# Kernel tuning notes

Measured on AMD Instinct MI355X. Metric: run time of the kernel, lower is better.

The kernel has to match this reference:

```python
import jax, jax.numpy as jnp
import numpy as np

N = 131072
IN, HID, OUT = 128, 256, 64
NUM_TASKS = 16
NUM_COPIES = 4
NUM_LAYERS = 3


def setup_inputs() -> dict:
    key = jax.random.key(0)
    ks = jax.random.split(key, 10)
    inputs = jax.random.normal(ks[0], (N, IN), dtype=jnp.float32)
    task_indices = jax.random.randint(ks[1], (N,), 0, NUM_TASKS, dtype=jnp.int32)
    copy_maps = jax.random.randint(ks[2], (NUM_LAYERS, NUM_TASKS), 0, NUM_COPIES, dtype=jnp.int32)
    # per-copy Linear weights, Kaiming-ish scale 1/sqrt(fan_in)
    W0 = jax.random.normal(ks[3], (NUM_COPIES, IN, HID), dtype=jnp.float32) / np.sqrt(IN)
    b0 = jax.random.normal(ks[4], (NUM_COPIES, HID), dtype=jnp.float32) * 0.01
    W1 = jax.random.normal(ks[5], (NUM_COPIES, HID, HID), dtype=jnp.float32) / np.sqrt(HID)
    b1 = jax.random.normal(ks[6], (NUM_COPIES, HID), dtype=jnp.float32) * 0.01
    W2 = jax.random.normal(ks[7], (NUM_COPIES, HID, OUT), dtype=jnp.float32) / np.sqrt(HID)
    b2 = jax.random.normal(ks[8], (NUM_COPIES, OUT), dtype=jnp.float32) * 0.01
    return {"inputs": inputs, "task_indices": task_indices, "copy_maps": copy_maps,
            "W0": W0, "b0": b0, "W1": W1, "b1": b1, "W2": W2, "b2": b2}


def _routed_layer(x, W, b, copy_idx, apply_tanh):
    # x: [N, d_in], W: [C, d_in, d_out], b: [C, d_out], copy_idx: [N]
    # Each token goes through exactly one copy's Linear. Equivalent to the
    # torch sort->per-copy-forward->unsort, expressed as masked accumulation
    # over the small fixed set of copies (avoids data-dependent shapes).
    y = jnp.zeros((x.shape[0], W.shape[2]), dtype=x.dtype)
    for c in range(W.shape[0]):
        mask = (copy_idx == c).astype(x.dtype)[:, None]  # [N, 1]
        y = y + mask * (x @ W[c] + b[c])
    return jnp.tanh(y) if apply_tanh else y


def reference(inputs, task_indices, copy_maps, W0, b0, W1, b1, W2, b2):
    x = inputs
    Ws = (W0, W1, W2)
    bs = (b0, b1, b2)
    for layer in range(NUM_LAYERS):
        copy_idx = copy_maps[layer][task_indices]  # [N] task->copy routing
        x = _routed_layer(x, Ws[layer], bs[layer], copy_idx,
                          apply_tanh=(layer != NUM_LAYERS - 1))
    return x
```

## Files before the change

### kernel.cpp

```cpp
#include <hip/hip_runtime.h>

#define N_TOK 131072
#define TILE 64
#define NT_MAX 2064

typedef __attribute__((ext_vector_type(8))) short s8v;
typedef __attribute__((ext_vector_type(4))) float f4v;
typedef unsigned short ushort_t;

__device__ __forceinline__ unsigned short f2bf(float x) {
    union { float f; unsigned u; } v; v.f = x;
    unsigned r = v.u + 0x7fffu + ((v.u >> 16) & 1u);
    return (unsigned short)(r >> 16);
}

__device__ __forceinline__ unsigned pk2(float a, float b) {
    union { float f; unsigned u; } x, y; x.f = a; y.f = b;
    return __byte_perm(x.u + 0x8000u, y.u + 0x8000u, 0x7632);
}

__device__ __forceinline__ float tanh_fast(float x) {
    float e = __expf(2.0f * x);
    float r = __builtin_amdgcn_rcpf(e + 1.0f);
    return __builtin_fmaf(-2.0f, r, 1.0f);
}

__global__ void prep_hist_kernel(const float* __restrict__ W0, const float* __restrict__ W1,
                                 const float* __restrict__ W2,
                                 ushort_t* __restrict__ W0p, ushort_t* __restrict__ W1p,
                                 ushort_t* __restrict__ W2p,
                                 const int* __restrict__ task, int* __restrict__ blockCounts) {
    if (blockIdx.x < 224) {
        int f = blockIdx.x * 256 + threadIdx.x;
        const float* src; ushort_t* dst; int K, N;
        if (f < 16384)      { src = W0; dst = W0p; K = 128; N = 256; }
        else if (f < 49152) { src = W1; dst = W1p; K = 256; N = 256; f -= 16384; }
        else                { src = W2; dst = W2p; K = 256; N = 64;  f -= 49152; }
        int fpc = (N >> 4) * (K >> 5) * 64;
        int c = f / fpc, r = f % fpc;
        int lane = r & 63;
        int kt = (r >> 6) % (K >> 5);
        int ftile = (r >> 6) / (K >> 5);
        int n = ftile * 16 + (lane & 15);
        int kbase = kt * 32 + (lane >> 4) * 8;
        const float* s = src + (size_t)c * K * N + (size_t)kbase * N + n;
        s8v pk;
#pragma unroll
        for (int j = 0; j < 8; j++) pk[j] = (short)f2bf(s[(size_t)j * N]);
        *reinterpret_cast<s8v*>(dst + ((size_t)(c * fpc + r) << 3)) = pk;
    } else {
        __shared__ int cnt[16];
        int t = threadIdx.x;
        int hb = blockIdx.x - 224;
        if (t < 16) cnt[t] = 0;
        __syncthreads();
        int base = hb * 2048 + t;
#pragma unroll
        for (int i = 0; i < 8; i++) atomicAdd(&cnt[task[base + i * 256]], 1);
        __syncthreads();
        if (t < 16) blockCounts[hb * 16 + t] = cnt[t];
    }
}

__global__ void sort_kernel(const int* __restrict__ task, const int* __restrict__ blockCounts,
                            int* __restrict__ tileTask, int* __restrict__ nT,
                            int* __restrict__ perm) {
    __shared__ int cntLds[1024];
    __shared__ int total[16], pref[16], rank[16];
    __shared__ int tokBase[16], tbase[17];
    int t = threadIdx.x, b = blockIdx.x;
    for (int i = t; i < 1024; i += 256) cntLds[i] = blockCounts[i];
    if (t < 16) rank[t] = 0;
    __syncthreads();
    if (t < 16) {
        int tot = 0, pf = 0;
#pragma unroll
        for (int bb = 0; bb < 64; bb++) {
            int v = cntLds[bb * 16 + t];
            tot += v;
            if (bb < b) pf += v;
        }
        total[t] = tot; pref[t] = pf;
    }
    __syncthreads();
    if (t == 0) {
        int tok = 0, tile = 0;
        for (int k = 0; k < 16; k++) {
            tokBase[k] = tok;
            tbase[k] = tile;
            int ntk = (total[k] + TILE - 1) / TILE;
            tok += ntk * TILE;
            tile += ntk;
        }
        tbase[16] = tile;
        if (b == 0) nT[0] = tile;
    }
    __syncthreads();
    if (b == 0) {
        for (int i = t; i < NT_MAX; i += 256) {
            int tk = 0;
            if (i < tbase[16]) {
#pragma unroll
                for (int k = 0; k < 16; k++) if (i >= tbase[k]) tk = k;
            }
            tileTask[i] = tk;
        }
        for (int i = t; i < 16 * TILE; i += 256) {
            int k = i >> 6, off = i & (TILE - 1);
            int idx = total[k] + off;
            int lim = ((total[k] + TILE - 1) / TILE) * TILE;
            if (idx < lim) perm[tokBase[k] + idx] = -1;
        }
    }
    int tk[8], my[8];
#pragma unroll
    for (int i = 0; i < 8; i++) {
        int idx = b * 2048 + i * 256 + t;
        tk[i] = task[idx];
        my[i] = atomicAdd(&rank[tk[i]], 1);
    }
#pragma unroll
    for (int i = 0; i < 8; i++) {
        int idx = b * 2048 + i * 256 + t;
        perm[tokBase[tk[i]] + pref[tk[i]] + my[i]] = idx;
    }
}

__launch_bounds__(512, 4)
__global__ void mlp_kernel(const float* __restrict__ x_in,
                           const int* __restrict__ cmap,
                           const float* __restrict__ b0,
                           const float* __restrict__ b1,
                           const float* __restrict__ b2,
                           const ushort_t* __restrict__ W0p,
                           const ushort_t* __restrict__ W1p,
                           const ushort_t* __restrict__ W2p,
                           const int* __restrict__ tileTask,
                           const int* __restrict__ nTp,
                           const int* __restrict__ perm,
                           float* __restrict__ out) {
    __shared__ __align__(16) ushort_t H1[16384];
    __shared__ __align__(16) ushort_t XH2[16384];

    int b = blockIdx.x;
    if (b >= nTp[0]) return;
    int t = threadIdx.x;
    int task = tileTask[b];
    int c0 = cmap[task], c1 = cmap[16 + task], c2 = cmap[32 + task];

    int w = t >> 6;
    int lane = t & 63;
    int l15 = lane & 15, lq = lane >> 4;

    {
        int r = t >> 3, q = t & 7;
        int tok = perm[b * TILE + r];
        float4 v0 = make_float4(0.f, 0.f, 0.f, 0.f), v1 = v0, v2 = v0, v3 = v0;
        if ((unsigned)tok < (unsigned)N_TOK) {
            const float4* src = reinterpret_cast<const float4*>(x_in) + (size_t)tok * 32 + q * 4;
            v0 = src[0]; v1 = src[1]; v2 = src[2]; v3 = src[3];
        }
        int fragid = (r >> 4) * 4 + (q >> 1);
        int lp0 = (r & 15) + 16 * ((q & 1) * 2);
        uint4 pk0, pk1;
        pk0.x = pk2(v0.x, v0.y); pk0.y = pk2(v0.z, v0.w);
        pk0.z = pk2(v1.x, v1.y); pk0.w = pk2(v1.z, v1.w);
        pk1.x = pk2(v2.x, v2.y); pk1.y = pk2(v2.z, v2.w);
        pk1.z = pk2(v3.x, v3.y); pk1.w = pk2(v3.z, v3.w);
        *reinterpret_cast<uint4*>(&XH2[(fragid * 64 + lp0) << 3]) = pk0;
        *reinterpret_cast<uint4*>(&XH2[(fragid * 64 + lp0 + 16) << 3]) = pk1;
    }
    __syncthreads();

    {
        f4v acc[2][4];
#pragma unroll
        for (int mi = 0; mi < 2; mi++) {
            float4 bv = *reinterpret_cast<const float4*>(b0 + c0 * 256 + (2 * w + mi) * 16 + lq * 4);
#pragma unroll
            for (int nt = 0; nt < 4; nt++) {
                acc[mi][nt][0] = bv.x; acc[mi][nt][1] = bv.y;
                acc[mi][nt][2] = bv.z; acc[mi][nt][3] = bv.w;
            }
        }
        const ushort_t* Wc = W0p + (size_t)c0 * 32768;
#pragma unroll
        for (int kt = 0; kt < 4; kt++) {
            s8v wa[2];
#pragma unroll
            for (int mi = 0; mi < 2; mi++)
                wa[mi] = *reinterpret_cast<const s8v*>(Wc + ((((2 * w + mi) * 4 + kt) * 64 + lane) << 3));
            s8v xb[4];
#pragma unroll
            for (int nt = 0; nt < 4; nt++)
                xb[nt] = *reinterpret_cast<const s8v*>(&XH2[((nt * 4 + kt) * 64 + lane) << 3]);
#pragma unroll
            for (int mi = 0; mi < 2; mi++)
#pragma unroll
                for (int nt = 0; nt < 4; nt++)
                    acc[mi][nt] = __builtin_amdgcn_mfma_f32_16x16x32_bf16(wa[mi], xb[nt], acc[mi][nt], 0, 0, 0);
        }
#pragma unroll
        for (int mi = 0; mi < 2; mi++) {
            int ft = 2 * w + mi;
            int kt_h = ft >> 1;
            int lanep = l15 + 16 * ((ft & 1) * 2 + (lq >> 1));
            int j0 = (lq & 1) * 4;
#pragma unroll
            for (int nt = 0; nt < 4; nt++) {
                float t0 = tanh_fast(acc[mi][nt][0]);
                float t1 = tanh_fast(acc[mi][nt][1]);
                float t2 = tanh_fast(acc[mi][nt][2]);
                float t3 = tanh_fast(acc[mi][nt][3]);
                uint2 pk; pk.x = pk2(t0, t1); pk.y = pk2(t2, t3);
                *reinterpret_cast<uint2*>(&H1[(((nt * 8 + kt_h) * 64 + lanep) << 3) + j0]) = pk;
            }
        }
    }
    __syncthreads();

    {
        f4v acc[2][4];
#pragma unroll
        for (int mi = 0; mi < 2; mi++) {
            float4 bv = *reinterpret_cast<const float4*>(b1 + c1 * 256 + (2 * w + mi) * 16 + lq * 4);
#pragma unroll
            for (int nt = 0; nt < 4; nt++) {
                acc[mi][nt][0] = bv.x; acc[mi][nt][1] = bv.y;
                acc[mi][nt][2] = bv.z; acc[mi][nt][3] = bv.w;
            }
        }
        const ushort_t* Wc = W1p + (size_t)c1 * 65536;
#pragma unroll
        for (int kt = 0; kt < 8; kt++) {
            s8v wa[2];
#pragma unroll
            for (int mi = 0; mi < 2; mi++)
                wa[mi] = *reinterpret_cast<const s8v*>(Wc + ((((2 * w + mi) * 8 + kt) * 64 + lane) << 3));
            s8v xb[4];
#pragma unroll
            for (int nt = 0; nt < 4; nt++)
                xb[nt] = *reinterpret_cast<const s8v*>(&H1[((nt * 8 + kt) * 64 + lane) << 3]);
#pragma unroll
            for (int mi = 0; mi < 2; mi++)
#pragma unroll
                for (int nt = 0; nt < 4; nt++)
                    acc[mi][nt] = __builtin_amdgcn_mfma_f32_16x16x32_bf16(wa[mi], xb[nt], acc[mi][nt], 0, 0, 0);
        }
#pragma unroll
        for (int mi = 0; mi < 2; mi++) {
            int ft = 2 * w + mi;
            int kt_h = ft >> 1;
            int lanep = l15 + 16 * ((ft & 1) * 2 + (lq >> 1));
            int j0 = (lq & 1) * 4;
#pragma unroll
            for (int nt = 0; nt < 4; nt++) {
                float t0 = tanh_fast(acc[mi][nt][0]);
                float t1 = tanh_fast(acc[mi][nt][1]);
                float t2 = tanh_fast(acc[mi][nt][2]);
                float t3 = tanh_fast(acc[mi][nt][3]);
                uint2 pk; pk.x = pk2(t0, t1); pk.y = pk2(t2, t3);
                *reinterpret_cast<uint2*>(&XH2[(((nt * 8 + kt_h) * 64 + lanep) << 3) + j0]) = pk;
            }
        }
    }
    __syncthreads();

    {
        int mt = w & 3, ntb = (w >> 2) * 2;
        float4 bv = *reinterpret_cast<const float4*>(b2 + c2 * 64 + mt * 16 + lq * 4);
        f4v acc[2];
#pragma unroll
        for (int e = 0; e < 2; e++) {
            acc[e][0] = bv.x; acc[e][1] = bv.y; acc[e][2] = bv.z; acc[e][3] = bv.w;
        }
        const ushort_t* Wc = W2p + (size_t)c2 * 16384;
#pragma unroll
        for (int kt = 0; kt < 8; kt++) {
            s8v wa = *reinterpret_cast<const s8v*>(Wc + (((mt * 8 + kt) * 64 + lane) << 3));
#pragma unroll
            for (int e = 0; e < 2; e++) {
                s8v xb = *reinterpret_cast<const s8v*>(&XH2[(((ntb + e) * 8 + kt) * 64 + lane) << 3]);
                acc[e] = __builtin_amdgcn_mfma_f32_16x16x32_bf16(wa, xb, acc[e], 0, 0, 0);
            }
        }
#pragma unroll
        for (int e = 0; e < 2; e++) {
            int nt = ntb + e;
            int tok = perm[b * TILE + nt * 16 + l15];
            if ((unsigned)tok < (unsigned)N_TOK) {
                float4 o;
                o.x = acc[e][0]; o.y = acc[e][1]; o.z = acc[e][2]; o.w = acc[e][3];
                *reinterpret_cast<float4*>(out + (size_t)tok * 64 + mt * 16 + lq * 4) = o;
            }
        }
    }
}

extern "C" void kernel_launch(void* const* d_in, const int* in_sizes, int n_in,
                              void* d_out, int out_size, void* d_ws, size_t ws_size,
                              hipStream_t stream) {
    const float* inputs = (const float*)d_in[0];
    const int*   task   = (const int*)d_in[1];
    const int*   cmap   = (const int*)d_in[2];
    const float* W0     = (const float*)d_in[3];
    const float* b0     = (const float*)d_in[4];
    const float* W1     = (const float*)d_in[5];
    const float* b1     = (const float*)d_in[6];
    const float* W2     = (const float*)d_in[7];
    const float* b2     = (const float*)d_in[8];
    float* out = (float*)d_out;

    char* ws = (char*)d_ws;
    int* blockCounts = (int*)(ws + 0);
    int* nT          = (int*)(ws + 4096);
    int* tileTask    = (int*)(ws + 4160);
    int* perm        = (int*)(ws + 12416);
    ushort_t* W0p    = (ushort_t*)(ws + 540800);
    ushort_t* W1p    = (ushort_t*)(ws + 802944);
    ushort_t* W2p    = (ushort_t*)(ws + 1327232);

    prep_hist_kernel<<<288, 256, 0, stream>>>(W0, W1, W2, W0p, W1p, W2p, task, blockCounts);
    sort_kernel<<<64, 256, 0, stream>>>(task, blockCounts, tileTask, nT, perm);
    mlp_kernel<<<NT_MAX, 512, 0, stream>>>(inputs, cmap, b0, b1, b2,
                                           W0p, W1p, W2p, tileTask, nT, perm, out);
}
```

Baseline: 162.2 us.

## Make MLP kernel persistent per task with register-resident weights and prefetch

The MLP kernel changes from one block per 64-token tile to 256 persistent blocks, 16 per task, each looping over that task's tiles with stride 16. All three layers' weight fragments and biases are loaded into registers once per block, and the next tile's input rows are prefetched while the current tile is being computed. The sort kernel now writes only per-task tile bases instead of a per-tile task table. This removes repeated weight reloads from global/L2 for every tile, at the cost of many more registers (launch bounds lowered to 2 blocks per CU) and possible load imbalance across tasks of unequal size.

```diff
diff --git a/kernel.cpp b/kernel.cpp
--- a/kernel.cpp
+++ b/kernel.cpp
@@ -3,6 +3,7 @@
 #define N_TOK 131072
 #define TILE 64
 #define NT_MAX 2064
+#define NBLK 256
 
 typedef __attribute__((ext_vector_type(8))) short s8v;
 typedef __attribute__((ext_vector_type(4))) float f4v;
@@ -63,8 +64,7 @@
 }
 
 __global__ void sort_kernel(const int* __restrict__ task, const int* __restrict__ blockCounts,
-                            int* __restrict__ tileTask, int* __restrict__ nT,
-                            int* __restrict__ perm) {
+                            int* __restrict__ tbaseG, int* __restrict__ perm) {
     __shared__ int cntLds[1024];
     __shared__ int total[16], pref[16], rank[16];
     __shared__ int tokBase[16], tbase[17];
@@ -93,18 +93,10 @@
             tile += ntk;
         }
         tbase[16] = tile;
-        if (b == 0) nT[0] = tile;
     }
     __syncthreads();
     if (b == 0) {
-        for (int i = t; i < NT_MAX; i += 256) {
-            int tk = 0;
-            if (i < tbase[16]) {
-#pragma unroll
-                for (int k = 0; k < 16; k++) if (i >= tbase[k]) tk = k;
-            }
-            tileTask[i] = tk;
-        }
+        if (t < 17) tbaseG[t] = tbase[t];
         for (int i = t; i < 16 * TILE; i += 256) {
             int k = i >> 6, off = i & (TILE - 1);
             int idx = total[k] + off;
@@ -126,7 +118,7 @@
     }
 }
 
-__launch_bounds__(512, 4)
+__launch_bounds__(512, 2)
 __global__ void mlp_kernel(const float* __restrict__ x_in,
                            const int* __restrict__ cmap,
                            const float* __restrict__ b0,
@@ -135,165 +127,202 @@
                            const ushort_t* __restrict__ W0p,
                            const ushort_t* __restrict__ W1p,
                            const ushort_t* __restrict__ W2p,
-                           const int* __restrict__ tileTask,
-                           const int* __restrict__ nTp,
+                           const int* __restrict__ tbaseG,
                            const int* __restrict__ perm,
                            float* __restrict__ out) {
     __shared__ __align__(16) ushort_t H1[16384];
     __shared__ __align__(16) ushort_t XH2[16384];
 
-    int b = blockIdx.x;
-    if (b >= nTp[0]) return;
+    int p = blockIdx.x;
+    int k = p >> 4, sub = p & 15;
+    int tBeg = tbaseG[k], tEnd = tbaseG[k + 1];
+    if (tBeg + sub >= tEnd) return;
+
     int t = threadIdx.x;
-    int task = tileTask[b];
-    int c0 = cmap[task], c1 = cmap[16 + task], c2 = cmap[32 + task];
+    int c0 = cmap[k], c1 = cmap[16 + k], c2 = cmap[32 + k];
 
     int w = t >> 6;
     int lane = t & 63;
     int l15 = lane & 15, lq = lane >> 4;
-
+    int mt2 = w & 3, ntb2 = (w >> 2) * 2;
+
+    s8v wa0[2][4], wa1[2][8], wa2r[8];
     {
-        int r = t >> 3, q = t & 7;
-        int tok = perm[b * TILE + r];
-        float4 v0 = make_float4(0.f, 0.f, 0.f, 0.f), v1 = v0, v2 = v0, v3 = v0;
-        if ((unsigned)tok < (unsigned)N_TOK) {
-            const float4* src = reinterpret_cast<const float4*>(x_in) + (size_t)tok * 32 + q * 4;
+        const ushort_t* Wc = W0p + (size_t)c0 * 32768;
+#pragma unroll
+        for (int mi = 0; mi < 2; mi++)
+#pragma unroll
+            for (int kt = 0; kt < 4; kt++)
+                wa0[mi][kt] = *reinterpret_cast<const s8v*>(Wc + ((((2 * w + mi) * 4 + kt) * 64 + lane) << 3));
+    }
+    {
+        const ushort_t* Wc = W1p + (size_t)c1 * 65536;
+#pragma unroll
+        for (int mi = 0; mi < 2; mi++)
+#pragma unroll
+            for (int kt = 0; kt < 8; kt++)
+                wa1[mi][kt] = *reinterpret_cast<const s8v*>(Wc + ((((2 * w + mi) * 8 + kt) * 64 + lane) << 3));
+    }
+    {
+        const ushort_t* Wc = W2p + (size_t)c2 * 16384;
+#pragma unroll
+        for (int kt = 0; kt < 8; kt++)
+            wa2r[kt] = *reinterpret_cast<const s8v*>(Wc + (((mt2 * 8 + kt) * 64 + lane) << 3));
+    }
+    float4 bv0[2], bv1[2], bv2;
+#pragma unroll
+    for (int mi = 0; mi < 2; mi++) {
+        bv0[mi] = *reinterpret_cast<const float4*>(b0 + c0 * 256 + (2 * w + mi) * 16 + lq * 4);
+        bv1[mi] = *reinterpret_cast<const float4*>(b1 + c1 * 256 + (2 * w + mi) * 16 + lq * 4);
+    }
+    bv2 = *reinterpret_cast<const float4*>(b2 + c2 * 64 + mt2 * 16 + lq * 4);
+
+    int r = t >> 3, q = t & 7;
+    const float4* xbase = reinterpret_cast<const float4*>(x_in);
+    float4 v0 = make_float4(0.f, 0.f, 0.f, 0.f), v1 = v0, v2 = v0, v3 = v0;
+    int ptok = -1;
+
+    int tile = tBeg + sub;
+    {
+        ptok = perm[tile * TILE + r];
+        if ((unsigned)ptok < (unsigned)N_TOK) {
+            const float4* src = xbase + (size_t)ptok * 32 + q * 4;
             v0 = src[0]; v1 = src[1]; v2 = src[2]; v3 = src[3];
         }
-        int fragid = (r >> 4) * 4 + (q >> 1);
-        int lp0 = (r & 15) + 16 * ((q & 1) * 2);
-        uint4 pk0, pk1;
-        pk0.x = pk2(v0.x, v0.y); pk0.y = pk2(v0.z, v0.w);
-        pk0.z = pk2(v1.x, v1.y); pk0.w = pk2(v1.z, v1.w);
-        pk1.x = pk2(v2.x, v2.y); pk1.y = pk2(v2.z, v2.w);
-        pk1.z = pk2(v3.x, v3.y); pk1.w = pk2(v3.z, v3.w);
-        *reinterpret_cast<uint4*>(&XH2[(fragid * 64 + lp0) << 3]) = pk0;
-        *reinterpret_cast<uint4*>(&XH2[(fragid * 64 + lp0 + 16) << 3]) = pk1;
-    }
-    __syncthreads();
-
-    {
-        f4v acc[2][4];
-#pragma unroll
-        for (int mi = 0; mi < 2; mi++) {
-            float4 bv = *reinterpret_cast<const float4*>(b0 + c0 * 256 + (2 * w + mi) * 16 + lq * 4);
-#pragma unroll
-            for (int nt = 0; nt < 4; nt++) {
-                acc[mi][nt][0] = bv.x; acc[mi][nt][1] = bv.y;
-                acc[mi][nt][2] = bv.z; acc[mi][nt][3] = bv.w;
-            }
-        }
-        const ushort_t* Wc = W0p + (size_t)c0 * 32768;
-#pragma unroll
-        for (int kt = 0; kt < 4; kt++) {
-            s8v wa[2];
+    }
+
+    for (; tile < tEnd; tile += 16) {
+        {
+            int fragid = (r >> 4) * 4 + (q >> 1);
+            int lp0 = (r & 15) + 16 * ((q & 1) * 2);
+            uint4 pk0, pk1;
+            pk0.x = pk2(v0.x, v0.y); pk0.y = pk2(v0.z, v0.w);
+            pk0.z = pk2(v1.x, v1.y); pk0.w = pk2(v1.z, v1.w);
+            pk1.x = pk2(v2.x, v2.y); pk1.y = pk2(v2.z, v2.w);
+            pk1.z = pk2(v3.x, v3.y); pk1.w = pk2(v3.z, v3.w);
+            *reinterpret_cast<uint4*>(&XH2[(fragid * 64 + lp0) << 3]) = pk0;
+            *reinterpret_cast<uint4*>(&XH2[(fragid * 64 + lp0 + 16) << 3]) = pk1;
+        }
+        int ntile = tile + 16;
+        if (ntile < tEnd) {
+            ptok = perm[ntile * TILE + r];
+            float4 z = make_float4(0.f, 0.f, 0.f, 0.f);
+            float4 a0 = z, a1 = z, a2 = z, a3 = z;
+            if ((unsigned)ptok < (unsigned)N_TOK) {
+                const float4* src = xbase + (size_t)ptok * 32 + q * 4;
+                a0 = src[0]; a1 = src[1]; a2 = src[2]; a3 = src[3];
+            }
+            v0 = a0; v1 = a1; v2 = a2; v3 = a3;
+        }
+        __syncthreads();
+
+        {
+            f4v acc[2][4];
 #pragma unroll
             for (int mi = 0; mi < 2; mi++)
-                wa[mi] = *reinterpret_cast<const s8v*>(Wc + ((((2 * w + mi) * 4 + kt) * 64 + lane) << 3));
-            s8v xb[4];
-#pragma unroll
-            for (int nt = 0; nt < 4; nt++)
-                xb[nt] = *reinterpret_cast<const s8v*>(&XH2[((nt * 4 + kt) * 64 + lane) << 3]);
+#pragma unroll
+                for (int nt = 0; nt < 4; nt++) {
+                    acc[mi][nt][0] = bv0[mi].x; acc[mi][nt][1] = bv0[mi].y;
+                    acc[mi][nt][2] = bv0[mi].z; acc[mi][nt][3] = bv0[mi].w;
+                }
+#pragma unroll
+            for (int kt = 0; kt < 4; kt++) {
+                s8v xb[4];
+#pragma unroll
+                for (int nt = 0; nt < 4; nt++)
+                    xb[nt] = *reinterpret_cast<const s8v*>(&XH2[((nt * 4 + kt) * 64 + lane) << 3]);
+#pragma unroll
+                for (int mi = 0; mi < 2; mi++)
+#pragma unroll
+                    for (int nt = 0; nt < 4; nt++)
+                        acc[mi][nt] = __builtin_amdgcn_mfma_f32_16x16x32_bf16(wa0[mi][kt], xb[nt], acc[mi][nt], 0, 0, 0);
+            }
+#pragma unroll
+            for (int mi = 0; mi < 2; mi++) {
+                int ft = 2 * w + mi;
+                int kt_h = ft >> 1;
+                int lanep = l15 + 16 * ((ft & 1) * 2 + (lq >> 1));
+                int j0 = (lq & 1) * 4;
+#pragma unroll
+                for (int nt = 0; nt < 4; nt++) {
+                    float t0 = tanh_fast(acc[mi][nt][0]);
+                    float t1 = tanh_fast(acc[mi][nt][1]);
+                    float t2 = tanh_fast(acc[mi][nt][2]);
+                    float t3 = tanh_fast(acc[mi][nt][3]);
+                    uint2 pk; pk.x = pk2(t0, t1); pk.y = pk2(t2, t3);
+                    *reinterpret_cast<uint2*>(&H1[(((nt * 8 + kt_h) * 64 + lanep) << 3) + j0]) = pk;
+                }
+            }
+        }
+        __syncthreads();
+
+        {
+            f4v acc[2][4];
 #pragma unroll
             for (int mi = 0; mi < 2; mi++)
 #pragma unroll
+                for (int nt = 0; nt < 4; nt++) {
+                    acc[mi][nt][0] = bv1[mi].x; acc[mi][nt][1] = bv1[mi].y;
+                    acc[mi][nt][2] = bv1[mi].z; acc[mi][nt][3] = bv1[mi].w;
+                }
+#pragma unroll
+            for (int kt = 0; kt < 8; kt++) {
+                s8v xb[4];
+#pragma unroll
                 for (int nt = 0; nt < 4; nt++)
-                    acc[mi][nt] = __builtin_amdgcn_mfma_f32_16x16x32_bf16(wa[mi], xb[nt], acc[mi][nt], 0, 0, 0);
-        }
-#pragma unroll
-        for (int mi = 0; mi < 2; mi++) {
-            int ft = 2 * w + mi;
-            int kt_h = ft >> 1;
-            int lanep = l15 + 16 * ((ft & 1) * 2 + (lq >> 1));
-            int j0 = (lq & 1) * 4;
-#pragma unroll
-            for (int nt = 0; nt < 4; nt++) {
-                float t0 = tanh_fast(acc[mi][nt][0]);
-                float t1 = tanh_fast(acc[mi][nt][1]);
-                float t2 = tanh_fast(acc[mi][nt][2]);
-                float t3 = tanh_fast(acc[mi][nt][3]);
-                uint2 pk; pk.x = pk2(t0, t1); pk.y = pk2(t2, t3);
-                *reinterpret_cast<uint2*>(&H1[(((nt * 8 + kt_h) * 64 + lanep) << 3) + j0]) = pk;
-            }
-        }
-    }
-    __syncthreads();
-
-    {
-        f4v acc[2][4];
-#pragma unroll
-        for (int mi = 0; mi < 2; mi++) {
-            float4 bv = *reinterpret_cast<const float4*>(b1 + c1 * 256 + (2 * w + mi) * 16 + lq * 4);
-#pragma unroll
-            for (int nt = 0; nt < 4; nt++) {
-                acc[mi][nt][0] = bv.x; acc[mi][nt][1] = bv.y;
-                acc[mi][nt][2] = bv.z; acc[mi][nt][3] = bv.w;
-            }
-        }
-        const ushort_t* Wc = W1p + (size_t)c1 * 65536;
-#pragma unroll
-        for (int kt = 0; kt < 8; kt++) {
-            s8v wa[2];
-#pragma unroll
-            for (int mi = 0; mi < 2; mi++)
-                wa[mi] = *reinterpret_cast<const s8v*>(Wc + ((((2 * w + mi) * 8 + kt) * 64 + lane) << 3));
-            s8v xb[4];
-#pragma unroll
-            for (int nt = 0; nt < 4; nt++)
-                xb[nt] = *reinterpret_cast<const s8v*>(&H1[((nt * 8 + kt) * 64 + lane) << 3]);
-#pragma unroll
-            for (int mi = 0; mi < 2; mi++)
-#pragma unroll
-                for (int nt = 0; nt < 4; nt++)
-                    acc[mi][nt] = __builtin_amdgcn_mfma_f32_16x16x32_bf16(wa[mi], xb[nt], acc[mi][nt], 0, 0, 0);
-        }
-#pragma unroll
-        for (int mi = 0; mi < 2; mi++) {
-            int ft = 2 * w + mi;
-            int kt_h = ft >> 1;
-            int lanep = l15 + 16 * ((ft & 1) * 2 + (lq >> 1));
-            int j0 = (lq & 1) * 4;
-#pragma unroll
-            for (int nt = 0; nt < 4; nt++) {
-                float t0 = tanh_fast(acc[mi][nt][0]);
-                float t1 = tanh_fast(acc[mi][nt][1]);
-                float t2 = tanh_fast(acc[mi][nt][2]);
-                float t3 = tanh_fast(acc[mi][nt][3]);
-                uint2 pk; pk.x = pk2(t0, t1); pk.y = pk2(t2, t3);
-                *reinterpret_cast<uint2*>(&XH2[(((nt * 8 + kt_h) * 64 + lanep) << 3) + j0]) = pk;
-            }
-        }
-    }
-    __syncthreads();
-
-    {
-        int mt = w & 3, ntb = (w >> 2) * 2;
-        float4 bv = *reinterpret_cast<const float4*>(b2 + c2 * 64 + mt * 16 + lq * 4);
-        f4v acc[2];
-#pragma unroll
-        for (int e = 0; e < 2; e++) {
-            acc[e][0] = bv.x; acc[e][1] = bv.y; acc[e][2] = bv.z; acc[e][3] = bv.w;
-        }
-        const ushort_t* Wc = W2p + (size_t)c2 * 16384;
-#pragma unroll
-        for (int kt = 0; kt < 8; kt++) {
-            s8v wa = *reinterpret_cast<const s8v*>(Wc + (((mt * 8 + kt) * 64 + lane) << 3));
+                    xb[nt] = *reinterpret_cast<const s8v*>(&H1[((nt * 8 + kt) * 64 + lane) << 3]);
+#pragma unroll
+                for (int mi = 0; mi < 2; mi++)
+#pragma unroll
+                    for (int nt = 0; nt < 4; nt++)
+                        acc[mi][nt] = __builtin_amdgcn_mfma_f32_16x16x32_bf16(wa1[mi][kt], xb[nt], acc[mi][nt], 0, 0, 0);
+            }
+#pragma unroll
+            for (int mi = 0; mi < 2; mi++) {
+                int ft = 2 * w + mi;
+                int kt_h = ft >> 1;
+                int lanep = l15 + 16 * ((ft & 1) * 2 + (lq >> 1));
+                int j0 = (lq & 1) * 4;
+#pragma unroll
+                for (int nt = 0; nt < 4; nt++) {
+                    float t0 = tanh_fast(acc[mi][nt][0]);
+                    float t1 = tanh_fast(acc[mi][nt][1]);
+                    float t2 = tanh_fast(acc[mi][nt][2]);
+                    float t3 = tanh_fast(acc[mi][nt][3]);
+                    uint2 pk; pk.x = pk2(t0, t1); pk.y = pk2(t2, t3);
+                    *reinterpret_cast<uint2*>(&XH2[(((nt * 8 + kt_h) * 64 + lanep) << 3) + j0]) = pk;
+                }
+            }
+        }
+        __syncthreads();
+
+        {
+            int tok0 = perm[tile * TILE + ntb2 * 16 + l15];
+            int tok1 = perm[tile * TILE + (ntb2 + 1) * 16 + l15];
+            f4v acc[2];
 #pragma unroll
             for (int e = 0; e < 2; e++) {
-                s8v xb = *reinterpret_cast<const s8v*>(&XH2[(((ntb + e) * 8 + kt) * 64 + lane) << 3]);
-                acc[e] = __builtin_amdgcn_mfma_f32_16x16x32_bf16(wa, xb, acc[e], 0, 0, 0);
-            }
-        }
-#pragma unroll
-        for (int e = 0; e < 2; e++) {
-            int nt = ntb + e;
-            int tok = perm[b * TILE + nt * 16 + l15];
-            if ((unsigned)tok < (unsigned)N_TOK) {
-                float4 o;
-                o.x = acc[e][0]; o.y = acc[e][1]; o.z = acc[e][2]; o.w = acc[e][3];
-                *reinterpret_cast<float4*>(out + (size_t)tok * 64 + mt * 16 + lq * 4) = o;
-            }
-        }
+                acc[e][0] = bv2.x; acc[e][1] = bv2.y; acc[e][2] = bv2.z; acc[e][3] = bv2.w;
+            }
+#pragma unroll
+            for (int kt = 0; kt < 8; kt++) {
+#pragma unroll
+                for (int e = 0; e < 2; e++) {
+                    s8v xb = *reinterpret_cast<const s8v*>(&XH2[(((ntb2 + e) * 8 + kt) * 64 + lane) << 3]);
+                    acc[e] = __builtin_amdgcn_mfma_f32_16x16x32_bf16(wa2r[kt], xb, acc[e], 0, 0, 0);
+                }
+            }
+#pragma unroll
+            for (int e = 0; e < 2; e++) {
+                int tok = e ? tok1 : tok0;
+                if ((unsigned)tok < (unsigned)N_TOK) {
+                    float4 o;
+                    o.x = acc[e][0]; o.y = acc[e][1]; o.z = acc[e][2]; o.w = acc[e][3];
+                    *reinterpret_cast<float4*>(out + (size_t)tok * 64 + mt2 * 16 + lq * 4) = o;
+                }
+            }
+        }
+        __syncthreads();
     }
 }
 
@@ -313,15 +342,14 @@
 
     char* ws = (char*)d_ws;
     int* blockCounts = (int*)(ws + 0);
-    int* nT          = (int*)(ws + 4096);
-    int* tileTask    = (int*)(ws + 4160);
-    int* perm        = (int*)(ws + 12416);
-    ushort_t* W0p    = (ushort_t*)(ws + 540800);
-    ushort_t* W1p    = (ushort_t*)(ws + 802944);
-    ushort_t* W2p    = (ushort_t*)(ws + 1327232);
+    int* tbaseG      = (int*)(ws + 4096);
+    int* perm        = (int*)(ws + 4224);
+    ushort_t* W0p    = (ushort_t*)(ws + 532608);
+    ushort_t* W1p    = (ushort_t*)(ws + 794752);
+    ushort_t* W2p    = (ushort_t*)(ws + 1319040);
 
     prep_hist_kernel<<<288, 256, 0, stream>>>(W0, W1, W2, W0p, W1p, W2p, task, blockCounts);
-    sort_kernel<<<64, 256, 0, stream>>>(task, blockCounts, tileTask, nT, perm);
-    mlp_kernel<<<NT_MAX, 512, 0, stream>>>(inputs, cmap, b0, b1, b2,
-                                           W0p, W1p, W2p, tileTask, nT, perm, out);
-}
+    sort_kernel<<<64, 256, 0, stream>>>(task, blockCounts, tbaseG, perm);
+    mlp_kernel<<<NBLK, 512, 0, stream>>>(inputs, cmap, b0, b1, b2,
+                                         W0p, W1p, W2p, tbaseG, perm, out);
+}
```

Result: no change. 160.5 us (-1.0%).

## Double token tile to 128 per block to halve weight refetches

Applied to the files above, without the earlier changes.

Raises the token tile from 64 to 128 rows per block, doubling the per-warp MFMA column tiles and LDS buffers to 64 KB each, and lowers launch bounds occupancy to 2. Each block now reuses every weight fragment across twice as many tokens, cutting global weight traffic and block count. It also switches tanh to use exp2 with a prescaled argument. The costs are higher register and LDS pressure, lower occupancy, and more padding waste per task segment.

```diff
diff --git a/kernel.cpp b/kernel.cpp
--- a/kernel.cpp
+++ b/kernel.cpp
@@ -1,8 +1,8 @@
 #include <hip/hip_runtime.h>
 
 #define N_TOK 131072
-#define TILE 64
-#define NT_MAX 2064
+#define TILE 128
+#define NT_MAX 1040
 
 typedef __attribute__((ext_vector_type(8))) short s8v;
 typedef __attribute__((ext_vector_type(4))) float f4v;
@@ -20,7 +20,7 @@
 }
 
 __device__ __forceinline__ float tanh_fast(float x) {
-    float e = __expf(2.0f * x);
+    float e = __builtin_amdgcn_exp2f(x * 2.8853900817779268f);
     float r = __builtin_amdgcn_rcpf(e + 1.0f);
     return __builtin_fmaf(-2.0f, r, 1.0f);
 }
@@ -106,7 +106,7 @@
             tileTask[i] = tk;
         }
         for (int i = t; i < 16 * TILE; i += 256) {
-            int k = i >> 6, off = i & (TILE - 1);
+            int k = i >> 7, off = i & (TILE - 1);
             int idx = total[k] + off;
             int lim = ((total[k] + TILE - 1) / TILE) * TILE;
             if (idx < lim) perm[tokBase[k] + idx] = -1;
@@ -126,7 +126,7 @@
     }
 }
 
-__launch_bounds__(512, 4)
+__launch_bounds__(512, 2)
 __global__ void mlp_kernel(const float* __restrict__ x_in,
                            const int* __restrict__ cmap,
                            const float* __restrict__ b0,
@@ -139,8 +139,8 @@
                            const int* __restrict__ nTp,
                            const int* __restrict__ perm,
                            float* __restrict__ out) {
-    __shared__ __align__(16) ushort_t H1[16384];
-    __shared__ __align__(16) ushort_t XH2[16384];
+    __shared__ __align__(16) ushort_t H1[32768];
+    __shared__ __align__(16) ushort_t XH2[32768];
 
     int b = blockIdx.x;
     if (b >= nTp[0]) return;
@@ -151,54 +151,54 @@
     int w = t >> 6;
     int lane = t & 63;
     int l15 = lane & 15, lq = lane >> 4;
+    int mt2 = w & 3, ntb2 = (w >> 2) * 4;
+
+    const ushort_t* Wc0 = W0p + (size_t)c0 * 32768;
+    const ushort_t* Wc1 = W1p + (size_t)c1 * 65536;
+    const ushort_t* Wc2 = W2p + (size_t)c2 * 16384;
 
     {
-        int r = t >> 3, q = t & 7;
+        int r = t >> 2, q = t & 3;
         int tok = perm[b * TILE + r];
-        float4 v0 = make_float4(0.f, 0.f, 0.f, 0.f), v1 = v0, v2 = v0, v3 = v0;
+        float4 v[8];
+#pragma unroll
+        for (int j = 0; j < 8; j++) v[j] = make_float4(0.f, 0.f, 0.f, 0.f);
         if ((unsigned)tok < (unsigned)N_TOK) {
-            const float4* src = reinterpret_cast<const float4*>(x_in) + (size_t)tok * 32 + q * 4;
-            v0 = src[0]; v1 = src[1]; v2 = src[2]; v3 = src[3];
-        }
-        int fragid = (r >> 4) * 4 + (q >> 1);
-        int lp0 = (r & 15) + 16 * ((q & 1) * 2);
-        uint4 pk0, pk1;
-        pk0.x = pk2(v0.x, v0.y); pk0.y = pk2(v0.z, v0.w);
-        pk0.z = pk2(v1.x, v1.y); pk0.w = pk2(v1.z, v1.w);
-        pk1.x = pk2(v2.x, v2.y); pk1.y = pk2(v2.z, v2.w);
-        pk1.z = pk2(v3.x, v3.y); pk1.w = pk2(v3.z, v3.w);
-        *reinterpret_cast<uint4*>(&XH2[(fragid * 64 + lp0) << 3]) = pk0;
-        *reinterpret_cast<uint4*>(&XH2[(fragid * 64 + lp0 + 16) << 3]) = pk1;
+            const float4* src = reinterpret_cast<const float4*>(x_in) + (size_t)tok * 32 + q * 8;
+#pragma unroll
+            for (int j = 0; j < 8; j++) v[j] = src[j];
+        }
+        int fbase = ((r >> 4) * 4 + q) * 64;
+#pragma unroll
+        for (int gq = 0; gq < 4; gq++) {
+            uint4 pk;
+            pk.x = pk2(v[2 * gq].x, v[2 * gq].y);     pk.y = pk2(v[2 * gq].z, v[2 * gq].w);
+            pk.z = pk2(v[2 * gq + 1].x, v[2 * gq + 1].y); pk.w = pk2(v[2 * gq + 1].z, v[2 * gq + 1].w);
+            *reinterpret_cast<uint4*>(&XH2[(fbase + (r & 15) + 16 * gq) << 3]) = pk;
+        }
     }
     __syncthreads();
 
     {
-        f4v acc[2][4];
+        f4v acc[2][8];
 #pragma unroll
         for (int mi = 0; mi < 2; mi++) {
-            float4 bv = *reinterpret_cast<const float4*>(b0 + c0 * 256 + (2 * w + mi) * 16 + lq * 4);
-#pragma unroll
-            for (int nt = 0; nt < 4; nt++) {
-                acc[mi][nt][0] = bv.x; acc[mi][nt][1] = bv.y;
-                acc[mi][nt][2] = bv.z; acc[mi][nt][3] = bv.w;
-            }
-        }
-        const ushort_t* Wc = W0p + (size_t)c0 * 32768;
+            f4v bv = *reinterpret_cast<const f4v*>(b0 + c0 * 256 + (2 * w + mi) * 16 + lq * 4);
+#pragma unroll
+            for (int nt = 0; nt < 8; nt++) acc[mi][nt] = bv;
+        }
 #pragma unroll
         for (int kt = 0; kt < 4; kt++) {
             s8v wa[2];
 #pragma unroll
             for (int mi = 0; mi < 2; mi++)
-                wa[mi] = *reinterpret_cast<const s8v*>(Wc + ((((2 * w + mi) * 4 + kt) * 64 + lane) << 3));
-            s8v xb[4];
-#pragma unroll
-            for (int nt = 0; nt < 4; nt++)
-                xb[nt] = *reinterpret_cast<const s8v*>(&XH2[((nt * 4 + kt) * 64 + lane) << 3]);
-#pragma unroll
-            for (int mi = 0; mi < 2; mi++)
-#pragma unroll
-                for (int nt = 0; nt < 4; nt++)
-                    acc[mi][nt] = __builtin_amdgcn_mfma_f32_16x16x32_bf16(wa[mi], xb[nt], acc[mi][nt], 0, 0, 0);
+                wa[mi] = *reinterpret_cast<const s8v*>(Wc0 + ((((2 * w + mi) * 4 + kt) * 64 + lane) << 3));
+#pragma unroll
+            for (int nt = 0; nt < 8; nt++) {
+                s8v xb = *reinterpret_cast<const s8v*>(&XH2[((nt * 4 + kt) * 64 + lane) << 3]);
+                acc[0][nt] = __builtin_amdgcn_mfma_f32_16x16x32_bf16(wa[0], xb, acc[0][nt], 0, 0, 0);
+                acc[1][nt] = __builtin_amdgcn_mfma_f32_16x16x32_bf16(wa[1], xb, acc[1][nt], 0, 0, 0);
+            }
         }
 #pragma unroll
         for (int mi = 0; mi < 2; mi++) {
@@ -207,7 +207,7 @@
             int lanep = l15 + 16 * ((ft & 1) * 2 + (lq >> 1));
             int j0 = (lq & 1) * 4;
 #pragma unroll
-            for (int nt = 0; nt < 4; nt++) {
+            for (int nt = 0; nt < 8; nt++) {
                 float t0 = tanh_fast(acc[mi][nt][0]);
                 float t1 = tanh_fast(acc[mi][nt][1]);
                 float t2 = tanh_fast(acc[mi][nt][2]);
@@ -220,32 +220,25 @@
     __syncthreads();
 
     {
-        f4v acc[2][4];
+        f4v acc[2][8];
 #pragma unroll
         for (int mi = 0; mi < 2; mi++) {
-            float4 bv = *reinterpret_cast<const float4*>(b1 + c1 * 256 + (2 * w + mi) * 16 + lq * 4);
-#pragma unroll
-            for (int nt = 0; nt < 4; nt++) {
-                acc[mi][nt][0] = bv.x; acc[mi][nt][1] = bv.y;
-                acc[mi][nt][2] = bv.z; acc[mi][nt][3] = bv.w;
-            }
-        }
-        const ushort_t* Wc = W1p + (size_t)c1 * 65536;
+            f4v bv = *reinterpret_cast<const f4v*>(b1 + c1 * 256 + (2 * w + mi) * 16 + lq * 4);
+#pragma unroll
+            for (int nt = 0; nt < 8; nt++) acc[mi][nt] = bv;
+        }
 #pragma unroll
         for (int kt = 0; kt < 8; kt++) {
             s8v wa[2];
 #pragma unroll
             for (int mi = 0; mi < 2; mi++)
-                wa[mi] = *reinterpret_cast<const s8v*>(Wc + ((((2 * w + mi) * 8 + kt) * 64 + lane) << 3));
-            s8v xb[4];
-#pragma unroll
-            for (int nt = 0; nt < 4; nt++)
-                xb[nt] = *reinterpret_cast<const s8v*>(&H1[((nt * 8 + kt) * 64 + lane) << 3]);
-#pragma unroll
-            for (int mi = 0; mi < 2; mi++)
-#pragma unroll
-                for (int nt = 0; nt < 4; nt++)
-                    acc[mi][nt] = __builtin_amdgcn_mfma_f32_16x16x32_bf16(wa[mi], xb[nt], acc[mi][nt], 0, 0, 0);
+                wa[mi] = *reinterpret_cast<const s8v*>(Wc1 + ((((2 * w + mi) * 8 + kt) * 64 + lane) << 3));
+#pragma unroll
+            for (int nt = 0; nt < 8; nt++) {
+                s8v xb = *reinterpret_cast<const s8v*>(&H1[((nt * 8 + kt) * 64 + lane) << 3]);
+                acc[0][nt] = __builtin_amdgcn_mfma_f32_16x16x32_bf16(wa[0], xb, acc[0][nt], 0, 0, 0);
+                acc[1][nt] = __builtin_amdgcn_mfma_f32_16x16x32_bf16(wa[1], xb, acc[1][nt], 0, 0, 0);
+            }
         }
 #pragma unroll
         for (int mi = 0; mi < 2; mi++) {
@@ -254,7 +247,7 @@
             int lanep = l15 + 16 * ((ft & 1) * 2 + (lq >> 1));
             int j0 = (lq & 1) * 4;
 #pragma unroll
-            for (int nt = 0; nt < 4; nt++) {
+            for (int nt = 0; nt < 8; nt++) {
                 float t0 = tanh_fast(acc[mi][nt][0]);
                 float t1 = tanh_fast(acc[mi][nt][1]);
                 float t2 = tanh_fast(acc[mi][nt][2]);
@@ -267,31 +260,26 @@
     __syncthreads();
 
     {
-        int mt = w & 3, ntb = (w >> 2) * 2;
-        float4 bv = *reinterpret_cast<const float4*>(b2 + c2 * 64 + mt * 16 + lq * 4);
-        f4v acc[2];
-#pragma unroll
-        for (int e = 0; e < 2; e++) {
-            acc[e][0] = bv.x; acc[e][1] = bv.y; acc[e][2] = bv.z; acc[e][3] = bv.w;
-        }
-        const ushort_t* Wc = W2p + (size_t)c2 * 16384;
+        f4v bv = *reinterpret_cast<const f4v*>(b2 + c2 * 64 + mt2 * 16 + lq * 4);
+        f4v acc[4];
+#pragma unroll
+        for (int e = 0; e < 4; e++) acc[e] = bv;
 #pragma unroll
         for (int kt = 0; kt < 8; kt++) {
-            s8v wa = *reinterpret_cast<const s8v*>(Wc + (((mt * 8 + kt) * 64 + lane) << 3));
-#pragma unroll
-            for (int e = 0; e < 2; e++) {
-                s8v xb = *reinterpret_cast<const s8v*>(&XH2[(((ntb + e) * 8 + kt) * 64 + lane) << 3]);
+            s8v wa = *reinterpret_cast<const s8v*>(Wc2 + (((mt2 * 8 + kt) * 64 + lane) << 3));
+#pragma unroll
+            for (int e = 0; e < 4; e++) {
+                s8v xb = *reinterpret_cast<const s8v*>(&XH2[(((ntb2 + e) * 8 + kt) * 64 + lane) << 3]);
                 acc[e] = __builtin_amdgcn_mfma_f32_16x16x32_bf16(wa, xb, acc[e], 0, 0, 0);
             }
         }
 #pragma unroll
-        for (int e = 0; e < 2; e++) {
-            int nt = ntb + e;
-            int tok = perm[b * TILE + nt * 16 + l15];
+        for (int e = 0; e < 4; e++) {
+            int tok = perm[b * TILE + (ntb2 + e) * 16 + l15];
             if ((unsigned)tok < (unsigned)N_TOK) {
                 float4 o;
                 o.x = acc[e][0]; o.y = acc[e][1]; o.z = acc[e][2]; o.w = acc[e][3];
-                *reinterpret_cast<float4*>(out + (size_t)tok * 64 + mt * 16 + lq * 4) = o;
+                *reinterpret_cast<float4*>(out + (size_t)tok * 64 + mt2 * 16 + lq * 4) = o;
             }
         }
     }
@@ -315,7 +303,7 @@
     int* blockCounts = (int*)(ws + 0);
     int* nT          = (int*)(ws + 4096);
     int* tileTask    = (int*)(ws + 4160);
-    int* perm        = (int*)(ws + 12416);
+    int* perm        = (int*)(ws + 8320);
     ushort_t* W0p    = (ushort_t*)(ws + 540800);
     ushort_t* W1p    = (ushort_t*)(ws + 802944);
     ushort_t* W2p    = (ushort_t*)(ws + 1327232);
```

New measurement: 181.4 us. +11.9%, slower.
